# Optimization experiments

Measured on AMD Instinct MI355X. Metric: run time of the kernel, lower is better.

## Reference

```python
import jax, jax.numpy as jnp
import numpy as np

N = 50000       # nodes
E = 800000      # edges (before self-loops)
F_IN = 128
HID = 64
HEADS = 4
OUT_DIM = 128
N_CLS = 2
NG = 500        # num graphs
SLOPE = 0.2     # GATConv leaky_relu negative slope
EPS = 1e-5      # BatchNorm eps


def setup_inputs() -> dict:
    key = jax.random.key(0)
    ks = jax.random.split(key, 24)
    s = 0.05
    d = {
        "x": jax.random.normal(ks[0], (N, F_IN), jnp.float32),
        "edge_index": jax.random.randint(ks[1], (2, E), 0, N, jnp.int64),
        "batch": jnp.sort(jax.random.randint(ks[2], (N,), 0, NG, jnp.int64)),
        # GATConv 1
        "W1": jax.random.normal(ks[3], (F_IN, HEADS * HID), jnp.float32) * s,
        "att_src1": jax.random.normal(ks[4], (HEADS, HID), jnp.float32) * s,
        "att_dst1": jax.random.normal(ks[5], (HEADS, HID), jnp.float32) * s,
        "b1": jnp.zeros((HEADS * HID,), jnp.float32),
        # BN1 (eval mode)
        "g1": jnp.ones((HEADS * HID,), jnp.float32),
        "be1": jnp.zeros((HEADS * HID,), jnp.float32),
        "rm1": jnp.zeros((HEADS * HID,), jnp.float32),
        "rv1": jnp.ones((HEADS * HID,), jnp.float32),
        # GATConv 2
        "W2": jax.random.normal(ks[6], (HEADS * HID, HEADS * HID), jnp.float32) * s,
        "att_src2": jax.random.normal(ks[7], (HEADS, HID), jnp.float32) * s,
        "att_dst2": jax.random.normal(ks[8], (HEADS, HID), jnp.float32) * s,
        "b2": jnp.zeros((HEADS * HID,), jnp.float32),
        # BN2 (eval mode)
        "g2": jnp.ones((HEADS * HID,), jnp.float32),
        "be2": jnp.zeros((HEADS * HID,), jnp.float32),
        "rm2": jnp.zeros((HEADS * HID,), jnp.float32),
        "rv2": jnp.ones((HEADS * HID,), jnp.float32),
        # MLP head
        "lw1": jax.random.normal(ks[9], (HEADS * HID, OUT_DIM), jnp.float32) * s,
        "lb1": jnp.zeros((OUT_DIM,), jnp.float32),
        "lw2": jax.random.normal(ks[10], (OUT_DIM, N_CLS), jnp.float32) * s,
        "lb2": jnp.zeros((N_CLS,), jnp.float32),
    }
    return d


def _gat_conv(x, src, dst, W, a_src, a_dst, b):
    """PyG GATConv (concat heads, add_self_loops=True, eval -> no dropout)."""
    n = x.shape[0]
    h = (x @ W).reshape(n, HEADS, -1)            # [N, H, C]
    loop = jnp.arange(n)
    s = jnp.concatenate([src, loop])             # self-loops appended
    d = jnp.concatenate([dst, loop])
    a_s = jnp.sum(h * a_src, axis=-1)            # [N, H]
    a_d = jnp.sum(h * a_dst, axis=-1)            # [N, H]
    e = jax.nn.leaky_relu(a_s[s] + a_d[d], SLOPE)   # [Et, H]
    # softmax over incoming edges per destination node
    m = jax.ops.segment_max(e, d, num_segments=n)
    ex = jnp.exp(e - m[d])
    denom = jax.ops.segment_sum(ex, d, num_segments=n)
    alpha = ex / denom[d]                        # [Et, H]
    msg = h[s] * alpha[:, :, None]               # [Et, H, C]
    out = jax.ops.segment_sum(msg, d, num_segments=n)
    return out.reshape(n, -1) + b


def _bn_eval(x, g, be, rm, rv):
    return (x - rm) * jax.lax.rsqrt(rv + EPS) * g + be


def reference(x, edge_index, batch, W1, att_src1, att_dst1, b1, g1, be1, rm1, rv1,
              W2, att_src2, att_dst2, b2, g2, be2, rm2, rv2, lw1, lb1, lw2, lb2):
    src, dst = edge_index[0], edge_index[1]
    h = jax.nn.relu(_gat_conv(x, src, dst, W1, att_src1, att_dst1, b1))
    h = _bn_eval(h, g1, be1, rm1, rv1)
    h = jax.nn.relu(_gat_conv(h, src, dst, W2, att_src2, att_dst2, b2))
    h = _bn_eval(h, g2, be2, rm2, rv2)
    # global mean pool over graphs
    sums = jax.ops.segment_sum(h, batch, num_segments=NG)
    cnt = jax.ops.segment_sum(jnp.ones((h.shape[0],), h.dtype), batch, num_segments=NG)
    pooled = sums / jnp.clip(cnt, 1.0)[:, None]
    z = jax.nn.relu(pooled @ lw1 + lb1)
    return z @ lw2 + lb2
```

## Files before the change

### kernel.cpp

```cpp
#include <hip/hip_runtime.h>
#include <hip/hip_bf16.h>
#include <math.h>

#define N_NODES 50000
#define M_PAD   50048
#define TILE_M  64
#define NBLK_GEMM (M_PAD / TILE_M)
#define N_EDGES 800000
#define EHALF   (N_EDGES / 2)
#define NBLK_BUILD ((EHALF + 255) / 256)
#define F_IN 128
#define HID 64
#define HEADS 4
#define FEAT 256
#define OUT_DIM 128
#define N_CLS 2
#define NG 500
#define SLOPE 0.2f
#define BN_EPS 1e-5f
#define ECAP 64

#define T_W1  (F_IN * 256)
#define T_W2  (FEAT * 256)
#define HPAD_ULL ((M_PAD - N_NODES) * FEAT / 4)
#define PREP_THREADS (T_W1 + T_W2 + HPAD_ULL + N_NODES)
#define NBLK_PREP ((PREP_THREADS + 255) / 256)

typedef __attribute__((ext_vector_type(8))) short short8;
typedef __attribute__((ext_vector_type(4))) float floatx4;
typedef __attribute__((ext_vector_type(2))) float floatx2;

__device__ inline unsigned short f2bf(float f) {
    unsigned int u = __float_as_uint(f);
    unsigned int lsb = (u >> 16) & 1u;
    return (unsigned short)((u + 0x7fffu + lsb) >> 16);
}

__global__ __launch_bounds__(256) void prep_small(
    const float* __restrict__ W1, const float* __restrict__ W2,
    unsigned short* __restrict__ W1T, unsigned short* __restrict__ W2T,
    unsigned short* __restrict__ h1bf,
    int* __restrict__ deg, int* __restrict__ ell, int* __restrict__ ovf_cnt) {
    int gid = blockIdx.x * 256 + threadIdx.x;
    if (gid < T_W1) {
        int k = gid >> 8, n = gid & 255;
        W1T[n * F_IN + k] = f2bf(W1[gid]);
        return;
    }
    int j = gid - T_W1;
    if (j < T_W2) {
        int k = j >> 8, n = j & 255;
        W2T[n * FEAT + k] = f2bf(W2[j]);
        return;
    }
    j -= T_W2;
    if (j < HPAD_ULL) {
        ((unsigned long long*)(h1bf + (size_t)N_NODES * FEAT))[j] = 0ULL;
        return;
    }
    j -= HPAD_ULL;
    if (j < N_NODES) {
        deg[j] = 1;
        ell[(size_t)j * ECAP] = j;
        if (j == 0) *ovf_cnt = 0;
    }
}

template<int K, bool AF32>
__device__ __forceinline__ void gemm_core(
    const void* __restrict__ Av, const unsigned short* __restrict__ BT,
    const float* __restrict__ att_src, const float* __restrict__ att_dst,
    unsigned char* __restrict__ h8, float* __restrict__ a_s,
    float* __restrict__ a_d, int bid, unsigned char* smem_raw) {
    constexpr int LS = 40;
    constexpr int C8 = 272;
    int t = threadIdx.x;
    unsigned short* As = (unsigned short*)smem_raw;
    unsigned short* Bs = As + TILE_M * LS;
    unsigned char*  s8 = smem_raw;
    int lane = t & 63, w = t >> 6;
    int row0 = bid * TILE_M;
    int mrow = lane & 15, quad = lane >> 4;

    floatx4 acc[4][4] = {};

    int rA = t >> 2, cA = (t & 3) * 8;

    const unsigned short* Ab = (const unsigned short*)Av;
    const float* Af = (const float*)Av;

    for (int k0 = 0; k0 < K; k0 += 32) {
        if (AF32) {
            uint4 pk = make_uint4(0, 0, 0, 0);
            if (row0 + rA < N_NODES) {
                float4 f0 = *(const float4*)&Af[(long long)(row0 + rA) * K + k0 + cA];
                float4 f1 = *(const float4*)&Af[(long long)(row0 + rA) * K + k0 + cA + 4];
                pk.x = (unsigned)f2bf(f0.x) | ((unsigned)f2bf(f0.y) << 16);
                pk.y = (unsigned)f2bf(f0.z) | ((unsigned)f2bf(f0.w) << 16);
                pk.z = (unsigned)f2bf(f1.x) | ((unsigned)f2bf(f1.y) << 16);
                pk.w = (unsigned)f2bf(f1.z) | ((unsigned)f2bf(f1.w) << 16);
            }
            *(uint4*)&As[rA * LS + cA] = pk;
        } else {
            *(uint4*)&As[rA * LS + cA] =
                *(const uint4*)&Ab[(long long)(row0 + rA) * K + k0 + cA];
        }
        #pragma unroll
        for (int j = 0; j < 4; j++) {
            int r = rA + j * 64;
            *(uint4*)&Bs[r * LS + cA] = *(const uint4*)&BT[(long long)r * K + k0 + cA];
        }
        __syncthreads();
        short8 bf[4];
        #pragma unroll
        for (int ni = 0; ni < 4; ni++)
            bf[ni] = *(const short8*)&Bs[(w * 64 + ni * 16 + mrow) * LS + quad * 8];
        #pragma unroll
        for (int mi = 0; mi < 4; mi++) {
            short8 af = *(const short8*)&As[(mi * 16 + mrow) * LS + quad * 8];
            #pragma unroll
            for (int ni = 0; ni < 4; ni++)
                acc[mi][ni] = __builtin_amdgcn_mfma_f32_16x16x32_bf16(af, bf[ni],
                                                                      acc[mi][ni], 0, 0, 0);
        }
        __syncthreads();
    }

    float ats[4], atd[4];
    #pragma unroll
    for (int ni = 0; ni < 4; ni++) {
        ats[ni] = att_src[w * 64 + ni * 16 + mrow];
        atd[ni] = att_dst[w * 64 + ni * 16 + mrow];
    }
    #pragma unroll
    for (int mi = 0; mi < 4; mi++) {
        #pragma unroll
        for (int r = 0; r < 4; r++) {
            int row = row0 + mi * 16 + quad * 4 + r;
            float ps = 0.f, pd = 0.f;
            #pragma unroll
            for (int ni = 0; ni < 4; ni++) {
                float v = acc[mi][ni][r];
                ps += v * ats[ni];
                pd += v * atd[ni];
            }
            #pragma unroll
            for (int off = 1; off < 16; off <<= 1) {
                ps += __shfl_xor(ps, off);
                pd += __shfl_xor(pd, off);
            }
            if (mrow == 0 && row < N_NODES) {
                a_s[row * 4 + w] = ps;
                a_d[row * 4 + w] = pd;
            }
        }
    }

    #pragma unroll
    for (int mi = 0; mi < 4; mi++)
        #pragma unroll
        for (int r = 0; r < 4; r++) {
            int row = mi * 16 + quad * 4 + r;
            #pragma unroll
            for (int ni = 0; ni < 4; ni += 2) {
                int pk = __builtin_amdgcn_cvt_pk_fp8_f32(acc[mi][ni][r],
                                                         acc[mi][ni + 1][r], 0, false);
                s8[row * C8 + w * 64 + ni * 16 + mrow]       = (unsigned char)(pk & 0xff);
                s8[row * C8 + w * 64 + (ni + 1) * 16 + mrow] = (unsigned char)((pk >> 8) & 0xff);
            }
        }
    __syncthreads();
    {
        int r2 = t >> 2, q = t & 3;
        const uint4* sp = (const uint4*)&s8[r2 * C8 + q * 64];
        uint4* dp = (uint4*)&h8[(long long)(row0 + r2) * FEAT + q * 64];
        #pragma unroll
        for (int k = 0; k < 4; k++)
            dp[k] = sp[k];
    }
}

__global__ __launch_bounds__(256, 4) void gemm1_build(
    const float* __restrict__ x, const unsigned short* __restrict__ BT,
    const float* __restrict__ att_src, const float* __restrict__ att_dst,
    unsigned char* __restrict__ h8, float* __restrict__ a_s,
    float* __restrict__ a_d,
    const int* __restrict__ src, const int* __restrict__ dst,
    int* __restrict__ deg, int* __restrict__ ell,
    int* __restrict__ ovf_cnt, int* __restrict__ ovf) {
    __shared__ __align__(16) unsigned char smem_raw[(TILE_M + FEAT) * 40 * 2];
    if (blockIdx.x >= NBLK_GEMM) {
        int i = (blockIdx.x - NBLK_GEMM) * 256 + threadIdx.x;
        if (i >= EHALF) return;
        int s0 = src[i],          d0 = dst[i];
        int s1 = src[i + EHALF],  d1 = dst[i + EHALF];
        int p0 = atomicAdd(&deg[d0], 1);
        int p1 = atomicAdd(&deg[d1], 1);
        if (p0 < ECAP) {
            ell[(size_t)d0 * ECAP + p0] = s0;
        } else {
            int k = atomicAdd(ovf_cnt, 1);
            ovf[2 * k] = s0; ovf[2 * k + 1] = d0;
        }
        if (p1 < ECAP) {
            ell[(size_t)d1 * ECAP + p1] = s1;
        } else {
            int k = atomicAdd(ovf_cnt, 1);
            ovf[2 * k] = s1; ovf[2 * k + 1] = d1;
        }
        return;
    }
    gemm_core<F_IN, true>(x, BT, att_src, att_dst, h8, a_s, a_d,
                          blockIdx.x, smem_raw);
}

__global__ __launch_bounds__(256, 4) void gemm2k(
    const unsigned short* __restrict__ Ab, const unsigned short* __restrict__ BT,
    const float* __restrict__ att_src, const float* __restrict__ att_dst,
    unsigned char* __restrict__ h8, float* __restrict__ a_s,
    float* __restrict__ a_d) {
    __shared__ __align__(16) unsigned char smem_raw[(TILE_M + FEAT) * 40 * 2];
    gemm_core<FEAT, false>(Ab, BT, att_src, att_dst, h8, a_s, a_d,
                           blockIdx.x, smem_raw);
}

__device__ __forceinline__ void gat_core(
    const int* __restrict__ deg_arr, const int* __restrict__ ell,
    const int* __restrict__ ovf_cnt, const int* __restrict__ ovf,
    const float* __restrict__ a_s, const float* __restrict__ a_d,
    const unsigned char* __restrict__ h8, const float* __restrict__ bias,
    const float* __restrict__ g, const float* __restrict__ be,
    const float* __restrict__ rm, const float* __restrict__ rv,
    unsigned short* __restrict__ out16) {
    int t = threadIdx.x;
    int lane = t & 63;
    int w = t >> 6;
    int hd = lane >> 4;
    int d = blockIdx.x * 4 + w;

    __shared__ float p_lds[4 * ECAP * 4];
    __shared__ int   o_lds[4 * ECAP];
    float* pw = &p_lds[w * ECAP * 4];
    int*   ow = &o_lds[w * ECAP];

    const unsigned int* __restrict__ H1 = (const unsigned int*)h8;

    int deg = deg_arr[d];
    float4 ad4 = *(const float4*)&a_d[d * 4];

    float den = 0.f;
    float4 acc = make_float4(0.f, 0.f, 0.f, 0.f);

    if (deg <= ECAP) {
        float lg[4] = {-INFINITY, -INFINITY, -INFINITY, -INFINITY};
        int s = 0;
        if (lane < deg) {
            s = ell[(size_t)d * ECAP + lane];
            float4 as4 = *(const float4*)&a_s[s * 4];
            float e0 = as4.x + ad4.x; lg[0] = e0 > 0.f ? e0 : SLOPE * e0;
            float e1 = as4.y + ad4.y; lg[1] = e1 > 0.f ? e1 : SLOPE * e1;
            float e2 = as4.z + ad4.z; lg[2] = e2 > 0.f ? e2 : SLOPE * e2;
            float e3 = as4.w + ad4.w; lg[3] = e3 > 0.f ? e3 : SLOPE * e3;
        }
        ow[lane] = s * 64;
        float mm = fmaxf(fmaxf(lg[0], lg[1]), fmaxf(lg[2], lg[3]));
        #pragma unroll
        for (int off = 1; off < 64; off <<= 1) mm = fmaxf(mm, __shfl_xor(mm, off));
        float4 pq = make_float4(0.f, 0.f, 0.f, 0.f);
        if (lane < deg) {
            pq.x = __expf(lg[0] - mm);
            pq.y = __expf(lg[1] - mm);
            pq.z = __expf(lg[2] - mm);
            pq.w = __expf(lg[3] - mm);
        }
        *(float4*)&pw[lane * 4] = pq;
        int deg4 = (deg + 3) & ~3;
        int cu[4];
        #pragma unroll
        for (int j = 0; j < 4; j++) cu[j] = (int)H1[ow[j] + lane];
        for (int e = 0; e < deg4; e += 4) {
            int nu[4] = {0, 0, 0, 0};
            if (e + 4 < deg4) {
                #pragma unroll
                for (int j = 0; j < 4; j++) nu[j] = (int)H1[ow[e + 4 + j] + lane];
            }
            #pragma unroll
            for (int j = 0; j < 4; j++) {
                float pj = pw[(e + j) * 4 + hd];
                den += pj;
                floatx2 lo = __builtin_amdgcn_cvt_pk_f32_fp8(cu[j], false);
                floatx2 hi = __builtin_amdgcn_cvt_pk_f32_fp8(cu[j], true);
                acc.x += pj * lo.x; acc.y += pj * lo.y;
                acc.z += pj * hi.x; acc.w += pj * hi.y;
            }
            #pragma unroll
            for (int j = 0; j < 4; j++) cu[j] = nu[j];
        }
    } else {
        float m_old;
        {
            int s = ell[(size_t)d * ECAP + lane];
            ow[lane] = s * 64;
            float4 as4 = *(const float4*)&a_s[s * 4];
            float lg[4];
            float e0 = as4.x + ad4.x; lg[0] = e0 > 0.f ? e0 : SLOPE * e0;
            float e1 = as4.y + ad4.y; lg[1] = e1 > 0.f ? e1 : SLOPE * e1;
            float e2 = as4.z + ad4.z; lg[2] = e2 > 0.f ? e2 : SLOPE * e2;
            float e3 = as4.w + ad4.w; lg[3] = e3 > 0.f ? e3 : SLOPE * e3;
            float mm = fmaxf(fmaxf(lg[0], lg[1]), fmaxf(lg[2], lg[3]));
            #pragma unroll
            for (int off = 1; off < 64; off <<= 1) mm = fmaxf(mm, __shfl_xor(mm, off));
            m_old = mm;
            float4 pq;
            pq.x = __expf(lg[0] - mm);
            pq.y = __expf(lg[1] - mm);
            pq.z = __expf(lg[2] - mm);
            pq.w = __expf(lg[3] - mm);
            *(float4*)&pw[lane * 4] = pq;
            for (int e = 0; e < ECAP; e++) {
                int oA = ow[e];
                float pA = pw[e * 4 + hd];
                int uA = (int)H1[oA + lane];
                den += pA;
                floatx2 a0 = __builtin_amdgcn_cvt_pk_f32_fp8(uA, false);
                floatx2 a1 = __builtin_amdgcn_cvt_pk_f32_fp8(uA, true);
                acc.x += pA * a0.x; acc.y += pA * a0.y;
                acc.z += pA * a1.x; acc.w += pA * a1.y;
            }
        }
        int nov = *ovf_cnt;
        for (int i = 0; i < nov; i++) {
            int s2 = ovf[2 * i], d2 = ovf[2 * i + 1];
            if (d2 != d) continue;
            float4 as4 = *(const float4*)&a_s[s2 * 4];
            float lg[4];
            float e0 = as4.x + ad4.x; lg[0] = e0 > 0.f ? e0 : SLOPE * e0;
            float e1 = as4.y + ad4.y; lg[1] = e1 > 0.f ? e1 : SLOPE * e1;
            float e2 = as4.z + ad4.z; lg[2] = e2 > 0.f ? e2 : SLOPE * e2;
            float e3 = as4.w + ad4.w; lg[3] = e3 > 0.f ? e3 : SLOPE * e3;
            float mmax = fmaxf(fmaxf(lg[0], lg[1]), fmaxf(lg[2], lg[3]));
            float m_new = fmaxf(m_old, mmax);
            float alpha = __expf(m_old - m_new);
            m_old = m_new;
            float ph = __expf(lg[hd] - m_new);
            acc.x *= alpha; acc.y *= alpha; acc.z *= alpha; acc.w *= alpha;
            den = den * alpha + ph;
            int u = (int)H1[s2 * 64 + lane];
            floatx2 a0 = __builtin_amdgcn_cvt_pk_f32_fp8(u, false);
            floatx2 a1 = __builtin_amdgcn_cvt_pk_f32_fp8(u, true);
            acc.x += ph * a0.x; acc.y += ph * a0.y;
            acc.z += ph * a1.x; acc.w += ph * a1.y;
        }
    }
    float inv = 1.f / den;
    int c0 = lane * 4;
    float4 bi = *(const float4*)&bias[c0];
    float4 gg = *(const float4*)&g[c0];
    float4 bb = *(const float4*)&be[c0];
    float4 mm4 = *(const float4*)&rm[c0];
    float4 vv = *(const float4*)&rv[c0];
    float v0 = fmaxf(acc.x * inv + bi.x, 0.f);
    float v1 = fmaxf(acc.y * inv + bi.y, 0.f);
    float v2 = fmaxf(acc.z * inv + bi.z, 0.f);
    float v3 = fmaxf(acc.w * inv + bi.w, 0.f);
    v0 = (v0 - mm4.x) * rsqrtf(vv.x + BN_EPS) * gg.x + bb.x;
    v1 = (v1 - mm4.y) * rsqrtf(vv.y + BN_EPS) * gg.y + bb.y;
    v2 = (v2 - mm4.z) * rsqrtf(vv.z + BN_EPS) * gg.z + bb.z;
    v3 = (v3 - mm4.w) * rsqrtf(vv.w + BN_EPS) * gg.w + bb.w;
    unsigned long long o =
        (unsigned long long)f2bf(v0) |
        ((unsigned long long)f2bf(v1) << 16) |
        ((unsigned long long)f2bf(v2) << 32) |
        ((unsigned long long)f2bf(v3) << 48);
    __builtin_nontemporal_store(o, (unsigned long long*)&out16[(long long)d * FEAT + c0]);
}

__global__ __launch_bounds__(256) void gat1(
    const int* __restrict__ deg_arr, const int* __restrict__ ell,
    const int* __restrict__ ovf_cnt, const int* __restrict__ ovf,
    const float* __restrict__ a_s, const float* __restrict__ a_d,
    const unsigned char* __restrict__ h8, const float* __restrict__ bias,
    const float* __restrict__ g, const float* __restrict__ be,
    const float* __restrict__ rm, const float* __restrict__ rv,
    unsigned short* __restrict__ out16) {
    gat_core(deg_arr, ell, ovf_cnt, ovf, a_s, a_d, h8, bias, g, be, rm, rv, out16);
}

__global__ __launch_bounds__(256) void gat2(
    const int* __restrict__ deg_arr, const int* __restrict__ ell,
    const int* __restrict__ ovf_cnt, const int* __restrict__ ovf,
    const float* __restrict__ a_s, const float* __restrict__ a_d,
    const unsigned char* __restrict__ h8, const float* __restrict__ bias,
    const float* __restrict__ g, const float* __restrict__ be,
    const float* __restrict__ rm, const float* __restrict__ rv,
    unsigned short* __restrict__ out16) {
    gat_core(deg_arr, ell, ovf_cnt, ovf, a_s, a_d, h8, bias, g, be, rm, rv, out16);
}

__global__ __launch_bounds__(256) void head_fused(
    const unsigned short* __restrict__ h2, const int* __restrict__ batch,
    const float* __restrict__ lw1, const float* __restrict__ lb1,
    const float* __restrict__ lw2, const float* __restrict__ lb2,
    float* __restrict__ out) {
    int gph = blockIdx.x;
    int t = threadIdx.x;
    __shared__ float pooled[FEAT];
    __shared__ float zl[OUT_DIM];
    __shared__ int lo_s, hi_s;
    if (t == 0) {
        int lo = 0, hi = N_NODES;
        while (lo < hi) { int mid = (lo + hi) >> 1; if (batch[mid] < gph) lo = mid + 1; else hi = mid; }
        lo_s = lo;
        int lo2 = 0, hi2 = N_NODES;
        while (lo2 < hi2) { int mid = (lo2 + hi2) >> 1; if (batch[mid] < gph + 1) lo2 = mid + 1; else hi2 = mid; }
        hi_s = lo2;
    }
    __syncthreads();
    int lo = lo_s, hi = hi_s;
    float a0 = 0.f, a1 = 0.f, a2 = 0.f, a3 = 0.f;
    int n = lo;
    for (; n + 3 < hi; n += 4) {
        a0 += __uint_as_float((unsigned)h2[(long long)n * FEAT + t] << 16);
        a1 += __uint_as_float((unsigned)h2[(long long)(n + 1) * FEAT + t] << 16);
        a2 += __uint_as_float((unsigned)h2[(long long)(n + 2) * FEAT + t] << 16);
        a3 += __uint_as_float((unsigned)h2[(long long)(n + 3) * FEAT + t] << 16);
    }
    for (; n < hi; n++) a0 += __uint_as_float((unsigned)h2[(long long)n * FEAT + t] << 16);
    float cnt = fmaxf((float)(hi - lo), 1.f);
    pooled[t] = (a0 + a1 + a2 + a3) / cnt;
    __syncthreads();
    int j = t >> 1, kh = t & 1;
    float zp = 0.f;
    #pragma unroll 8
    for (int k = kh * 128; k < kh * 128 + 128; k++)
        zp += pooled[k] * lw1[k * OUT_DIM + j];
    zp += __shfl_xor(zp, 1);
    if (kh == 0) zl[j] = fmaxf(zp + lb1[j], 0.f);
    __syncthreads();
    int w = t >> 6, lane = t & 63;
    if (w < 2) {
        float p = zl[lane] * lw2[lane * 2 + w] + zl[lane + 64] * lw2[(lane + 64) * 2 + w];
        #pragma unroll
        for (int off = 1; off < 64; off <<= 1) p += __shfl_xor(p, off);
        if (lane == 0) out[gph * 2 + w] = p + lb2[w];
    }
}

extern "C" void kernel_launch(void* const* d_in, const int* in_sizes, int n_in,
                              void* d_out, int out_size, void* d_ws, size_t ws_size,
                              hipStream_t stream) {
    const float* x       = (const float*)d_in[0];
    const int*   ei      = (const int*)d_in[1];
    const int*   batch   = (const int*)d_in[2];
    const float* W1      = (const float*)d_in[3];
    const float* att_s1  = (const float*)d_in[4];
    const float* att_d1  = (const float*)d_in[5];
    const float* b1      = (const float*)d_in[6];
    const float* g1      = (const float*)d_in[7];
    const float* be1     = (const float*)d_in[8];
    const float* rm1     = (const float*)d_in[9];
    const float* rv1     = (const float*)d_in[10];
    const float* W2      = (const float*)d_in[11];
    const float* att_s2  = (const float*)d_in[12];
    const float* att_d2  = (const float*)d_in[13];
    const float* b2      = (const float*)d_in[14];
    const float* g2      = (const float*)d_in[15];
    const float* be2     = (const float*)d_in[16];
    const float* rm2     = (const float*)d_in[17];
    const float* rv2     = (const float*)d_in[18];
    const float* lw1     = (const float*)d_in[19];
    const float* lb1     = (const float*)d_in[20];
    const float* lw2     = (const float*)d_in[21];
    const float* lb2     = (const float*)d_in[22];
    float* out           = (float*)d_out;

    const int* src = ei;
    const int* dst = ei + N_EDGES;

    char* p = (char*)d_ws;
    auto carve = [&p](size_t bytes) -> void* {
        void* r = (void*)p;
        p += (bytes + 63) & ~(size_t)63;
        return r;
    };
    unsigned short* h2bf = (unsigned short*)carve(sizeof(short) * (size_t)N_NODES * FEAT);
    float* a_s    = (float*)carve(sizeof(float) * N_NODES * HEADS);
    float* a_d    = (float*)carve(sizeof(float) * N_NODES * HEADS);
    int*   deg    = (int*)carve(sizeof(int) * N_NODES);
    int*   ovf_cnt= (int*)carve(sizeof(int) * 16);
    int*   ell    = (int*)carve(sizeof(int) * (size_t)N_NODES * ECAP);
    int*   ovf    = (int*)carve(sizeof(int) * 2 * (N_EDGES + N_NODES));
    unsigned char*  h8   = (unsigned char*)carve((size_t)M_PAD * FEAT);
    unsigned short* h1bf = (unsigned short*)carve(sizeof(short) * (size_t)M_PAD * FEAT);
    unsigned short* w1t  = (unsigned short*)carve(sizeof(short) * FEAT * F_IN);
    unsigned short* w2t  = (unsigned short*)carve(sizeof(short) * FEAT * FEAT);

    prep_small<<<NBLK_PREP, 256, 0, stream>>>(
        W1, W2, w1t, w2t, h1bf, deg, ell, ovf_cnt);

    gemm1_build<<<NBLK_GEMM + NBLK_BUILD, 256, 0, stream>>>(
        x, w1t, att_s1, att_d1, h8, a_s, a_d,
        src, dst, deg, ell, ovf_cnt, ovf);
    gat1<<<N_NODES / 4, 256, 0, stream>>>(deg, ell, ovf_cnt, ovf, a_s, a_d, h8,
                                          b1, g1, be1, rm1, rv1, h1bf);

    gemm2k<<<NBLK_GEMM, 256, 0, stream>>>(
        h1bf, w2t, att_s2, att_d2, h8, a_s, a_d);
    gat2<<<N_NODES / 4, 256, 0, stream>>>(deg, ell, ovf_cnt, ovf, a_s, a_d, h8,
                                          b2, g2, be2, rm2, rv2, h2bf);

    head_fused<<<NG, 256, 0, stream>>>(h2bf, batch, lw1, lb1, lw2, lb2, out);
}
```

Before: 300.1 us.

## Load GEMM fragments directly from global, handle self-loop implicitly, shrink prep kernel

The GEMM core no longer stages A and B tiles through LDS. Each wave now loads its MFMA fragments straight from global memory, which removes two barriers per k-step and shrinks shared memory. Self-loops are no longer written into the ELL lists: degree starts at zero via memset and the self edge is handled inside the aggregation. The W2 transpose moves into the gemm1/build launch, so the prep kernel only converts W1. The risks are redundant, uncoalesced global loads across waves (each wave reloads A rows) and extra memset launches.

```diff
diff --git a/kernel.cpp b/kernel.cpp
--- a/kernel.cpp
+++ b/kernel.cpp
@@ -21,10 +21,9 @@
 #define ECAP 64
 
 #define T_W1  (F_IN * 256)
+#define NBLK_W1 (T_W1 / 256)
 #define T_W2  (FEAT * 256)
-#define HPAD_ULL ((M_PAD - N_NODES) * FEAT / 4)
-#define PREP_THREADS (T_W1 + T_W2 + HPAD_ULL + N_NODES)
-#define NBLK_PREP ((PREP_THREADS + 255) / 256)
+#define NBLK_W2T (T_W2 / 256)
 
 typedef __attribute__((ext_vector_type(8))) short short8;
 typedef __attribute__((ext_vector_type(4))) float floatx4;
@@ -36,34 +35,11 @@
     return (unsigned short)((u + 0x7fffu + lsb) >> 16);
 }
 
-__global__ __launch_bounds__(256) void prep_small(
-    const float* __restrict__ W1, const float* __restrict__ W2,
-    unsigned short* __restrict__ W1T, unsigned short* __restrict__ W2T,
-    unsigned short* __restrict__ h1bf,
-    int* __restrict__ deg, int* __restrict__ ell, int* __restrict__ ovf_cnt) {
+__global__ __launch_bounds__(256) void prep_w1(
+    const float* __restrict__ W1, unsigned short* __restrict__ W1T) {
     int gid = blockIdx.x * 256 + threadIdx.x;
-    if (gid < T_W1) {
-        int k = gid >> 8, n = gid & 255;
-        W1T[n * F_IN + k] = f2bf(W1[gid]);
-        return;
-    }
-    int j = gid - T_W1;
-    if (j < T_W2) {
-        int k = j >> 8, n = j & 255;
-        W2T[n * FEAT + k] = f2bf(W2[j]);
-        return;
-    }
-    j -= T_W2;
-    if (j < HPAD_ULL) {
-        ((unsigned long long*)(h1bf + (size_t)N_NODES * FEAT))[j] = 0ULL;
-        return;
-    }
-    j -= HPAD_ULL;
-    if (j < N_NODES) {
-        deg[j] = 1;
-        ell[(size_t)j * ECAP] = j;
-        if (j == 0) *ovf_cnt = 0;
-    }
+    int k = gid >> 8, n = gid & 255;
+    W1T[n * F_IN + k] = f2bf(W1[gid]);
 }
 
 template<int K, bool AF32>
@@ -71,59 +47,47 @@
     const void* __restrict__ Av, const unsigned short* __restrict__ BT,
     const float* __restrict__ att_src, const float* __restrict__ att_dst,
     unsigned char* __restrict__ h8, float* __restrict__ a_s,
-    float* __restrict__ a_d, int bid, unsigned char* smem_raw) {
-    constexpr int LS = 40;
+    float* __restrict__ a_d, int bid, unsigned char* s8) {
     constexpr int C8 = 272;
     int t = threadIdx.x;
-    unsigned short* As = (unsigned short*)smem_raw;
-    unsigned short* Bs = As + TILE_M * LS;
-    unsigned char*  s8 = smem_raw;
     int lane = t & 63, w = t >> 6;
     int row0 = bid * TILE_M;
     int mrow = lane & 15, quad = lane >> 4;
 
     floatx4 acc[4][4] = {};
 
-    int rA = t >> 2, cA = (t & 3) * 8;
-
     const unsigned short* Ab = (const unsigned short*)Av;
     const float* Af = (const float*)Av;
 
     for (int k0 = 0; k0 < K; k0 += 32) {
-        if (AF32) {
-            uint4 pk = make_uint4(0, 0, 0, 0);
-            if (row0 + rA < N_NODES) {
-                float4 f0 = *(const float4*)&Af[(long long)(row0 + rA) * K + k0 + cA];
-                float4 f1 = *(const float4*)&Af[(long long)(row0 + rA) * K + k0 + cA + 4];
-                pk.x = (unsigned)f2bf(f0.x) | ((unsigned)f2bf(f0.y) << 16);
-                pk.y = (unsigned)f2bf(f0.z) | ((unsigned)f2bf(f0.w) << 16);
-                pk.z = (unsigned)f2bf(f1.x) | ((unsigned)f2bf(f1.y) << 16);
-                pk.w = (unsigned)f2bf(f1.z) | ((unsigned)f2bf(f1.w) << 16);
-            }
-            *(uint4*)&As[rA * LS + cA] = pk;
-        } else {
-            *(uint4*)&As[rA * LS + cA] =
-                *(const uint4*)&Ab[(long long)(row0 + rA) * K + k0 + cA];
-        }
-        #pragma unroll
-        for (int j = 0; j < 4; j++) {
-            int r = rA + j * 64;
-            *(uint4*)&Bs[r * LS + cA] = *(const uint4*)&BT[(long long)r * K + k0 + cA];
-        }
-        __syncthreads();
         short8 bf[4];
         #pragma unroll
         for (int ni = 0; ni < 4; ni++)
-            bf[ni] = *(const short8*)&Bs[(w * 64 + ni * 16 + mrow) * LS + quad * 8];
+            bf[ni] = *(const short8*)&BT[(long long)(w * 64 + ni * 16 + mrow) * K
+                                         + k0 + quad * 8];
         #pragma unroll
         for (int mi = 0; mi < 4; mi++) {
-            short8 af = *(const short8*)&As[(mi * 16 + mrow) * LS + quad * 8];
+            int row = row0 + mi * 16 + mrow;
+            short8 af;
+            if (AF32) {
+                uint4 pk = make_uint4(0, 0, 0, 0);
+                if (row < N_NODES) {
+                    float4 f0 = *(const float4*)&Af[(long long)row * K + k0 + quad * 8];
+                    float4 f1 = *(const float4*)&Af[(long long)row * K + k0 + quad * 8 + 4];
+                    pk.x = (unsigned)f2bf(f0.x) | ((unsigned)f2bf(f0.y) << 16);
+                    pk.y = (unsigned)f2bf(f0.z) | ((unsigned)f2bf(f0.w) << 16);
+                    pk.z = (unsigned)f2bf(f1.x) | ((unsigned)f2bf(f1.y) << 16);
+                    pk.w = (unsigned)f2bf(f1.z) | ((unsigned)f2bf(f1.w) << 16);
+                }
+                af = *(short8*)&pk;
+            } else {
+                af = *(const short8*)&Ab[(long long)row * K + k0 + quad * 8];
+            }
             #pragma unroll
             for (int ni = 0; ni < 4; ni++)
                 acc[mi][ni] = __builtin_amdgcn_mfma_f32_16x16x32_bf16(af, bf[ni],
                                                                       acc[mi][ni], 0, 0, 0);
         }
-        __syncthreads();
     }
 
     float ats[4], atd[4];
@@ -182,15 +146,17 @@
 
 __global__ __launch_bounds__(256, 4) void gemm1_build(
     const float* __restrict__ x, const unsigned short* __restrict__ BT,
+    const float* __restrict__ W2, unsigned short* __restrict__ W2T,
     const float* __restrict__ att_src, const float* __restrict__ att_dst,
     unsigned char* __restrict__ h8, float* __restrict__ a_s,
     float* __restrict__ a_d,
     const int* __restrict__ src, const int* __restrict__ dst,
     int* __restrict__ deg, int* __restrict__ ell,
     int* __restrict__ ovf_cnt, int* __restrict__ ovf) {
-    __shared__ __align__(16) unsigned char smem_raw[(TILE_M + FEAT) * 40 * 2];
-    if (blockIdx.x >= NBLK_GEMM) {
-        int i = (blockIdx.x - NBLK_GEMM) * 256 + threadIdx.x;
+    __shared__ __align__(16) unsigned char smem_raw[TILE_M * 272];
+    int bid = blockIdx.x;
+    if (bid >= NBLK_GEMM + NBLK_W2T) {
+        int i = (bid - NBLK_GEMM - NBLK_W2T) * 256 + threadIdx.x;
         if (i >= EHALF) return;
         int s0 = src[i],          d0 = dst[i];
         int s1 = src[i + EHALF],  d1 = dst[i + EHALF];
@@ -210,8 +176,13 @@
         }
         return;
     }
-    gemm_core<F_IN, true>(x, BT, att_src, att_dst, h8, a_s, a_d,
-                          blockIdx.x, smem_raw);
+    if (bid >= NBLK_GEMM) {
+        int j = (bid - NBLK_GEMM) * 256 + threadIdx.x;
+        int k = j >> 8, n = j & 255;
+        W2T[n * FEAT + k] = f2bf(W2[j]);
+        return;
+    }
+    gemm_core<F_IN, true>(x, BT, att_src, att_dst, h8, a_s, a_d, bid, smem_raw);
 }
 
 __global__ __launch_bounds__(256, 4) void gemm2k(
@@ -219,7 +190,7 @@
     const float* __restrict__ att_src, const float* __restrict__ att_dst,
     unsigned char* __restrict__ h8, float* __restrict__ a_s,
     float* __restrict__ a_d) {
-    __shared__ __align__(16) unsigned char smem_raw[(TILE_M + FEAT) * 40 * 2];
+    __shared__ __align__(16) unsigned char smem_raw[TILE_M * 272];
     gemm_core<FEAT, false>(Ab, BT, att_src, att_dst, h8, a_s, a_d,
                            blockIdx.x, smem_raw);
 }
@@ -245,17 +216,18 @@
 
     const unsigned int* __restrict__ H1 = (const unsigned int*)h8;
 
-    int deg = deg_arr[d];
+    int degr = deg_arr[d];
     float4 ad4 = *(const float4*)&a_d[d * 4];
 
     float den = 0.f;
     float4 acc = make_float4(0.f, 0.f, 0.f, 0.f);
 
-    if (deg <= ECAP) {
+    if (degr < ECAP) {
+        int tot = degr + 1;
         float lg[4] = {-INFINITY, -INFINITY, -INFINITY, -INFINITY};
-        int s = 0;
-        if (lane < deg) {
-            s = ell[(size_t)d * ECAP + lane];
+        int s = d;
+        if (lane < degr) s = ell[(size_t)d * ECAP + lane];
+        if (lane < tot) {
             float4 as4 = *(const float4*)&a_s[s * 4];
             float e0 = as4.x + ad4.x; lg[0] = e0 > 0.f ? e0 : SLOPE * e0;
             float e1 = as4.y + ad4.y; lg[1] = e1 > 0.f ? e1 : SLOPE * e1;
@@ -267,14 +239,14 @@
         #pragma unroll
         for (int off = 1; off < 64; off <<= 1) mm = fmaxf(mm, __shfl_xor(mm, off));
         float4 pq = make_float4(0.f, 0.f, 0.f, 0.f);
-        if (lane < deg) {
+        if (lane < tot) {
             pq.x = __expf(lg[0] - mm);
             pq.y = __expf(lg[1] - mm);
             pq.z = __expf(lg[2] - mm);
             pq.w = __expf(lg[3] - mm);
         }
         *(float4*)&pw[lane * 4] = pq;
-        int deg4 = (deg + 3) & ~3;
+        int deg4 = (tot + 3) & ~3;
         int cu[4];
         #pragma unroll
         for (int j = 0; j < 4; j++) cu[j] = (int)H1[ow[j] + lane];
@@ -327,6 +299,26 @@
                 acc.x += pA * a0.x; acc.y += pA * a0.y;
                 acc.z += pA * a1.x; acc.w += pA * a1.y;
             }
+        }
+        {
+            float4 as4 = *(const float4*)&a_s[d * 4];
+            float lg[4];
+            float e0 = as4.x + ad4.x; lg[0] = e0 > 0.f ? e0 : SLOPE * e0;
+            float e1 = as4.y + ad4.y; lg[1] = e1 > 0.f ? e1 : SLOPE * e1;
+            float e2 = as4.z + ad4.z; lg[2] = e2 > 0.f ? e2 : SLOPE * e2;
+            float e3 = as4.w + ad4.w; lg[3] = e3 > 0.f ? e3 : SLOPE * e3;
+            float mmax = fmaxf(fmaxf(lg[0], lg[1]), fmaxf(lg[2], lg[3]));
+            float m_new = fmaxf(m_old, mmax);
+            float alpha = __expf(m_old - m_new);
+            m_old = m_new;
+            float ph = __expf(lg[hd] - m_new);
+            acc.x *= alpha; acc.y *= alpha; acc.z *= alpha; acc.w *= alpha;
+            den = den * alpha + ph;
+            int u = (int)H1[d * 64 + lane];
+            floatx2 a0 = __builtin_amdgcn_cvt_pk_f32_fp8(u, false);
+            floatx2 a1 = __builtin_amdgcn_cvt_pk_f32_fp8(u, true);
+            acc.x += ph * a0.x; acc.y += ph * a0.y;
+            acc.z += ph * a1.x; acc.w += ph * a1.y;
         }
         int nov = *ovf_cnt;
         for (int i = 0; i < nov; i++) {
@@ -495,11 +487,14 @@
     unsigned short* w1t  = (unsigned short*)carve(sizeof(short) * FEAT * F_IN);
     unsigned short* w2t  = (unsigned short*)carve(sizeof(short) * FEAT * FEAT);
 
-    prep_small<<<NBLK_PREP, 256, 0, stream>>>(
-        W1, W2, w1t, w2t, h1bf, deg, ell, ovf_cnt);
-
-    gemm1_build<<<NBLK_GEMM + NBLK_BUILD, 256, 0, stream>>>(
-        x, w1t, att_s1, att_d1, h8, a_s, a_d,
+    hipMemsetAsync(deg, 0, sizeof(int) * N_NODES + 64, stream);
+    hipMemsetAsync(h1bf + (size_t)N_NODES * FEAT, 0,
+                   sizeof(short) * (size_t)(M_PAD - N_NODES) * FEAT, stream);
+
+    prep_w1<<<NBLK_W1, 256, 0, stream>>>(W1, w1t);
+
+    gemm1_build<<<NBLK_GEMM + NBLK_W2T + NBLK_BUILD, 256, 0, stream>>>(
+        x, w1t, W2, w2t, att_s1, att_d1, h8, a_s, a_d,
         src, dst, deg, ell, ovf_cnt, ovf);
     gat1<<<N_NODES / 4, 256, 0, stream>>>(deg, ell, ovf_cnt, ovf, a_s, a_d, h8,
                                           b1, g1, be1, rm1, rv1, h1bf);
```

Measured after the change: 321.2 us. 7.0% more time.
